# Performance work log

Measured on AMD Instinct MI355X. Metric: run time of the kernel, lower is better.

Reference implementation:

```python
import jax, jax.numpy as jnp
import numpy as np

N_NODES = 100000
N_EDGES = 1600000
D_FEAT = 50
N_CLASSES = 47
K_HOPS = 2


def setup_inputs() -> dict:
    key = jax.random.key(0)
    k1, k2, k3, k4 = jax.random.split(key, 4)
    feat = jax.random.normal(k1, (N_NODES, D_FEAT), dtype=jnp.float32)
    edge_src = jax.random.randint(k2, (N_EDGES,), 0, N_NODES)
    edge_dst = jax.random.randint(k3, (N_EDGES,), 0, N_NODES)
    # xavier_uniform for fc.weight [n_classes, in_feats], zeros bias
    limit = np.sqrt(6.0 / (N_CLASSES + D_FEAT)).astype(np.float32)
    W = jax.random.uniform(k4, (N_CLASSES, D_FEAT), dtype=jnp.float32,
                           minval=-limit, maxval=limit)
    b = jnp.zeros((N_CLASSES,), dtype=jnp.float32)
    return {"feat": feat, "W": W, "b": b,
            "edge_src": edge_src, "edge_dst": edge_dst, "K": K_HOPS}


def reference(feat, W, b, edge_src, edge_dst, K):
    # S = D^-1/2 (A + I) D^-1/2 ; precompute = S^K ; out = (S^K feat) W^T + b
    N = feat.shape[0]
    ones = jnp.ones_like(edge_dst, dtype=feat.dtype)
    deg = 1.0 + jax.ops.segment_sum(ones, edge_dst, num_segments=N)  # row sums of A+I
    dinv = jax.lax.rsqrt(deg)                       # [N]
    w_e = dinv[edge_dst] * dinv[edge_src]           # [E] edge weights of S
    self_w = dinv * dinv                            # [N] self-loop weights (1/d)
    h = feat
    for _ in range(K):  # K hops: h <- S @ h
        msg = w_e[:, None] * h[edge_src]            # [E, D] gather + scale
        h = jax.ops.segment_sum(msg, edge_dst, num_segments=N) + self_w[:, None] * h
    return h @ W.T + b                              # [N, n_classes]
```

## Files before the change

kernel.cpp:

```cpp
#include <hip/hip_runtime.h>
#include <hip/hip_fp16.h>

#define NN 100000
#define NE 1600000
#define DF 50
#define NC 47
#define DP 64
#define ZROW NN
#define MAXDEG 48

static_assert(NN % 16 == 0, "grid exactness");
static_assert(NE % 4 == 0, "int4 edge loads");

typedef _Float16 half8 __attribute__((ext_vector_type(8)));
typedef float float4v __attribute__((ext_vector_type(4)));
typedef int int4v __attribute__((ext_vector_type(4)));

#define RCH_I4 800
#define NCHUNK (NE / 4 / RCH_I4)
static_assert((NE / 4) % RCH_I4 == 0, "chunk exactness");

__global__ __launch_bounds__(256) void slotscat_kernel(const int4v* __restrict__ src4,
                                                       const int4v* __restrict__ dst4,
                                                       unsigned* __restrict__ cursor,
                                                       int* __restrict__ cols) {
    int r = blockIdx.x & 7;
    int c = blockIdx.x >> 3;
    int base = c * RCH_I4;
    for (int i = threadIdx.x; i < RCH_I4; i += 256) {
        int4v s = __builtin_nontemporal_load(&src4[base + i]);
        int4v q = __builtin_nontemporal_load(&dst4[base + i]);
        #pragma unroll
        for (int k = 0; k < 4; ++k) {
            int d = q[k];
            if ((d & 7) == r) {
                unsigned p = atomicAdd(&cursor[d], 1u);
                if (p < MAXDEG) cols[d * MAXDEG + p] = s[k];
            }
        }
    }
}

__global__ void pad_kernel(const unsigned* __restrict__ deg, const float* __restrict__ f,
                           float* __restrict__ dinv, float* __restrict__ selfw,
                           float4* __restrict__ fp, float4* __restrict__ h1p4) {
    int t = blockIdx.x * blockDim.x + threadIdx.x;
    if (t >= (NN + 1) * 8) return;
    int n = t >> 3, c = t & 7;
    float r = 0.f;
    if (n < NN) r = rsqrtf(1.0f + (float)deg[n]);
    if (c == 0 && n < NN) {
        dinv[n]  = r;
        selfw[n] = r * r;
    }
    float v[8];
    #pragma unroll
    for (int i = 0; i < 8; ++i) {
        int e = c * 8 + i;
        v[i] = (n < NN && e < DF) ? r * f[n * DF + e] : 0.f;
    }
    float4 ov;
    __half2* op = (__half2*)&ov;
    #pragma unroll
    for (int i = 0; i < 4; ++i) op[i] = __floats2half2_rn(v[2 * i], v[2 * i + 1]);
    fp[t] = ov;
    if (n == NN) h1p4[t] = make_float4(0.f, 0.f, 0.f, 0.f);
}

__global__ __launch_bounds__(256) void hop_kernel(const _Float16* __restrict__ h,
    const int* __restrict__ cols, const unsigned* __restrict__ deg,
    const float* __restrict__ scaleArr, _Float16* __restrict__ hn) {

    int lane = threadIdx.x & 63;
    int wid  = (int)((blockIdx.x * blockDim.x + threadIdx.x) >> 6);
    int half = lane >> 5;
    int g    = (lane >> 3) & 3;
    int qid  = lane & 7;

    int nd = 2 * wid + half;
    unsigned rs = (unsigned)nd * MAXDEG;
    unsigned d  = min(deg[nd], (unsigned)MAXDEG);
    unsigned dmax = max(__shfl(d, 0), __shfl(d, 32));

    float acc[8] = {0.f, 0.f, 0.f, 0.f, 0.f, 0.f, 0.f, 0.f};

    auto body = [&](unsigned j) {
        int c = __builtin_nontemporal_load(&cols[rs + j]);
        c = (j < d) ? c : ZROW;
        half8 v = *(const half8*)(h + (unsigned)c * DP + qid * 8);
        #pragma unroll
        for (int i = 0; i < 8; ++i) acc[i] += (float)v[i];
    };

    for (unsigned j0 = 0; j0 < dmax; j0 += 32u) {
        #pragma unroll
        for (int u = 0; u < 4; ++u) body(j0 + (unsigned)(g + 4 * u));
        if (j0 + 16u < dmax) {
            #pragma unroll
            for (int u = 4; u < 8; ++u) body(j0 + (unsigned)(g + 4 * u));
        }
    }

    #pragma unroll
    for (int i = 0; i < 8; ++i) {
        acc[i] += __shfl_xor(acc[i], 8);
        acc[i] += __shfl_xor(acc[i], 16);
    }

    float s = scaleArr[nd];
    half8 hv = *(const half8*)(h + (unsigned)nd * DP + qid * 8);
    half8 ov;
    #pragma unroll
    for (int i = 0; i < 8; ++i)
        ov[i] = (_Float16)(s * (acc[i] + (float)hv[i]));
    if ((lane & 24) == 0)
        __builtin_nontemporal_store(ov, (half8*)(hn + (unsigned)nd * DP + qid * 8));
}

__global__ __launch_bounds__(256) void fc_kernel(const _Float16* __restrict__ h2,
    const float* __restrict__ W, const float* __restrict__ b,
    float* __restrict__ out, int MT) {

    __shared__ _Float16 sW[48 * 72];
    __shared__ float sB[48];

    for (int i = threadIdx.x; i < 48 * 64; i += 256) {
        int n = i >> 6, k = i & 63;
        float v = (n < NC && k < DF) ? W[n * DF + k] : 0.f;
        sW[n * 72 + k] = (_Float16)v;
    }
    if (threadIdx.x < 48) sB[threadIdx.x] = (threadIdx.x < NC) ? b[threadIdx.x] : 0.f;
    __syncthreads();

    int lane = threadIdx.x & 63;
    int wid  = (int)((blockIdx.x * blockDim.x + threadIdx.x) >> 6);
    if (wid >= MT) return;

    int m0 = wid * 16;
    int am = lane & 15;
    int aq = lane >> 4;

    const half8* arow = (const half8*)(h2 + (long)(m0 + am) * DP);
    half8 a0 = arow[aq];
    half8 a1 = arow[aq + 4];
    int row = aq * 4;

    #pragma unroll
    for (int t = 0; t < 3; ++t) {
        int n = t * 16 + am;
        const half8* brow = (const half8*)(sW + n * 72);
        half8 b0 = brow[aq];
        half8 b1 = brow[aq + 4];
        float4v c = {0.f, 0.f, 0.f, 0.f};
        c = __builtin_amdgcn_mfma_f32_16x16x32_f16(a0, b0, c, 0, 0, 0);
        c = __builtin_amdgcn_mfma_f32_16x16x32_f16(a1, b1, c, 0, 0, 0);
        if (n < NC) {
            float bn = sB[n];
            #pragma unroll
            for (int r = 0; r < 4; ++r)
                out[(long)(m0 + row + r) * NC + n] = c[r] + bn;
        }
    }
}

extern "C" void kernel_launch(void* const* d_in, const int* in_sizes, int n_in,
                              void* d_out, int out_size, void* d_ws, size_t ws_size,
                              hipStream_t stream) {
    const float* feat = (const float*)d_in[0];
    const float* W    = (const float*)d_in[1];
    const float* b    = (const float*)d_in[2];
    const int*  esrc  = (const int*)d_in[3];
    const int*  edst  = (const int*)d_in[4];
    float* out = (float*)d_out;

    char* ws = (char*)d_ws;
    unsigned* cursor = (unsigned*)ws; ws += NN * sizeof(unsigned);
    float*    dinv   = (float*)ws;    ws += NN * sizeof(float);
    float*    selfw  = (float*)ws;    ws += NN * sizeof(float);
    int*      cols   = (int*)ws;      ws += (size_t)NN * MAXDEG * sizeof(int);
    _Float16* featp  = (_Float16*)ws; ws += (size_t)(NN + 1) * DP * sizeof(_Float16);
    _Float16* h1p    = (_Float16*)ws; ws += (size_t)(NN + 1) * DP * sizeof(_Float16);
    _Float16* h2p    = (_Float16*)ws;

    hipMemsetAsync(cursor, 0, NN * sizeof(unsigned), stream);

    slotscat_kernel<<<8 * NCHUNK, 256, 0, stream>>>(
        (const int4v*)esrc, (const int4v*)edst, cursor, cols);

    pad_kernel<<<((NN + 1) * 8 + 255) / 256, 256, 0, stream>>>(
        cursor, feat, dinv, selfw, (float4*)featp, (float4*)h1p);

    const int hop_blocks = NN / 8;
    hop_kernel<<<hop_blocks, 256, 0, stream>>>(featp, cols, cursor, selfw, h1p);
    hop_kernel<<<hop_blocks, 256, 0, stream>>>(h1p, cols, cursor, dinv, h2p);

    const int MT = NN / 16;
    fc_kernel<<<(MT + 3) / 4, 256, 0, stream>>>(h2p, W, b, out, MT);
}
```

Measured before the change: 247.5 us.

## Build adjacency via two-pass LDS binning instead of global atomic scatter

The CSR-like adjacency build, which used global atomics per edge, is replaced by two passes. binA_kernel bins each edge chunk by destination range using shared-memory atomics into a bucket arena. slotB_kernel then slots each range's edges into cols with shared-memory atomics and writes the degrees, so the cursor memset is no longer needed. The edge arrays are read once instead of eight times. In exchange the scheme adds an extra launch and an intermediate arena that reuses the feature buffer's memory, and it silently drops edges if any bucket exceeds its fixed capacity.

```diff
diff --git a/kernel.cpp b/kernel.cpp
--- a/kernel.cpp
+++ b/kernel.cpp
@@ -9,35 +9,72 @@
 #define ZROW NN
 #define MAXDEG 48
 
+#define RB   128
+#define RSH  7
+#define RNG  782
+#define CCH  250
+#define CI4  (NE / 4 / CCH)
+#define BK   48
+
 static_assert(NN % 16 == 0, "grid exactness");
-static_assert(NE % 4 == 0, "int4 edge loads");
+static_assert((NE / 4) % CCH == 0, "chunk exactness");
 
 typedef _Float16 half8 __attribute__((ext_vector_type(8)));
 typedef float float4v __attribute__((ext_vector_type(4)));
 typedef int int4v __attribute__((ext_vector_type(4)));
 
-#define RCH_I4 800
-#define NCHUNK (NE / 4 / RCH_I4)
-static_assert((NE / 4) % RCH_I4 == 0, "chunk exactness");
-
-__global__ __launch_bounds__(256) void slotscat_kernel(const int4v* __restrict__ src4,
-                                                       const int4v* __restrict__ dst4,
-                                                       unsigned* __restrict__ cursor,
-                                                       int* __restrict__ cols) {
-    int r = blockIdx.x & 7;
-    int c = blockIdx.x >> 3;
-    int base = c * RCH_I4;
-    for (int i = threadIdx.x; i < RCH_I4; i += 256) {
+__global__ __launch_bounds__(256) void binA_kernel(const int4v* __restrict__ src4,
+                                                   const int4v* __restrict__ dst4,
+                                                   unsigned* __restrict__ arena,
+                                                   unsigned short* __restrict__ counts) {
+    __shared__ unsigned lcnt[RNG];
+    int c = blockIdx.x;
+    for (int i = threadIdx.x; i < RNG; i += 256) lcnt[i] = 0;
+    __syncthreads();
+    int base = c * CI4;
+    for (int i = threadIdx.x; i < CI4; i += 256) {
         int4v s = __builtin_nontemporal_load(&src4[base + i]);
         int4v q = __builtin_nontemporal_load(&dst4[base + i]);
         #pragma unroll
         for (int k = 0; k < 4; ++k) {
-            int d = q[k];
-            if ((d & 7) == r) {
-                unsigned p = atomicAdd(&cursor[d], 1u);
-                if (p < MAXDEG) cols[d * MAXDEG + p] = s[k];
-            }
-        }
+            unsigned d  = (unsigned)q[k];
+            unsigned r  = d >> RSH;
+            unsigned dl = d & (RB - 1);
+            unsigned p  = atomicAdd(&lcnt[r], 1u);
+            if (p < BK)
+                arena[((size_t)r * CCH + c) * BK + p] = (unsigned)s[k] | (dl << 17);
+        }
+    }
+    __syncthreads();
+    for (int i = threadIdx.x; i < RNG; i += 256)
+        counts[(size_t)c * RNG + i] = (unsigned short)min(lcnt[i], (unsigned)BK);
+}
+
+__global__ __launch_bounds__(256) void slotB_kernel(const unsigned* __restrict__ arena,
+                                                    const unsigned short* __restrict__ counts,
+                                                    int* __restrict__ cols,
+                                                    unsigned* __restrict__ deg) {
+    __shared__ unsigned lcur[RB];
+    int r = blockIdx.x;
+    if (threadIdx.x < RB) lcur[threadIdx.x] = 0;
+    __syncthreads();
+    int c = threadIdx.x;
+    if (c < CCH) {
+        int cnt = counts[(size_t)c * RNG + r];
+        const unsigned* bk = arena + ((size_t)r * CCH + c) * BK;
+        for (int j = 0; j < cnt; ++j) {
+            unsigned e    = bk[j];
+            unsigned srcv = e & 0x1FFFFu;
+            unsigned dl   = (e >> 17) & (RB - 1);
+            unsigned p    = atomicAdd(&lcur[dl], 1u);
+            if (p < MAXDEG)
+                cols[((size_t)r * RB + dl) * MAXDEG + p] = (int)srcv;
+        }
+    }
+    __syncthreads();
+    if (threadIdx.x < RB) {
+        int node = r * RB + threadIdx.x;
+        if (node < NN) deg[node] = lcur[threadIdx.x];
     }
 }
 
@@ -174,25 +211,26 @@
     float* out = (float*)d_out;
 
     char* ws = (char*)d_ws;
-    unsigned* cursor = (unsigned*)ws; ws += NN * sizeof(unsigned);
-    float*    dinv   = (float*)ws;    ws += NN * sizeof(float);
-    float*    selfw  = (float*)ws;    ws += NN * sizeof(float);
-    int*      cols   = (int*)ws;      ws += (size_t)NN * MAXDEG * sizeof(int);
-    _Float16* featp  = (_Float16*)ws; ws += (size_t)(NN + 1) * DP * sizeof(_Float16);
-    _Float16* h1p    = (_Float16*)ws; ws += (size_t)(NN + 1) * DP * sizeof(_Float16);
-    _Float16* h2p    = (_Float16*)ws;
-
-    hipMemsetAsync(cursor, 0, NN * sizeof(unsigned), stream);
-
-    slotscat_kernel<<<8 * NCHUNK, 256, 0, stream>>>(
-        (const int4v*)esrc, (const int4v*)edst, cursor, cols);
+    unsigned* deg    = (unsigned*)ws;       ws += ((size_t)NN * 4 + 127) & ~127ull;
+    float*    dinv   = (float*)ws;          ws += ((size_t)NN * 4 + 127) & ~127ull;
+    float*    selfw  = (float*)ws;          ws += ((size_t)NN * 4 + 127) & ~127ull;
+    int*      cols   = (int*)ws;            ws += ((size_t)NN * MAXDEG * 4 + 127) & ~127ull;
+    unsigned short* counts = (unsigned short*)ws; ws += ((size_t)CCH * RNG * 2 + 127) & ~127ull;
+    char* uni = ws;
+    unsigned* arena  = (unsigned*)uni;
+    _Float16* featp  = (_Float16*)uni;
+    _Float16* h1p    = featp + (size_t)(NN + 1) * DP;
+    _Float16* h2p    = h1p   + (size_t)(NN + 1) * DP;
+
+    binA_kernel<<<CCH, 256, 0, stream>>>((const int4v*)esrc, (const int4v*)edst, arena, counts);
+    slotB_kernel<<<RNG, 256, 0, stream>>>(arena, counts, cols, deg);
 
     pad_kernel<<<((NN + 1) * 8 + 255) / 256, 256, 0, stream>>>(
-        cursor, feat, dinv, selfw, (float4*)featp, (float4*)h1p);
+        deg, feat, dinv, selfw, (float4*)featp, (float4*)h1p);
 
     const int hop_blocks = NN / 8;
-    hop_kernel<<<hop_blocks, 256, 0, stream>>>(featp, cols, cursor, selfw, h1p);
-    hop_kernel<<<hop_blocks, 256, 0, stream>>>(h1p, cols, cursor, dinv, h2p);
+    hop_kernel<<<hop_blocks, 256, 0, stream>>>(featp, cols, deg, selfw, h1p);
+    hop_kernel<<<hop_blocks, 256, 0, stream>>>(h1p, cols, deg, dinv, h2p);
 
     const int MT = NN / 16;
     fc_kernel<<<(MT + 3) / 4, 256, 0, stream>>>(h2p, W, b, out, MT);
```

Result: faster. 220.8 us (-10.8%).
